# Performance work log

Hardware: AMD Instinct MI355X
Metric: run time of the kernel (lower is better)

## Reference

```python
import jax, jax.numpy as jnp
import numpy as np

B, S, D, H, E, KW = 2, 2048, 1024, 8, 128, 16  # batch, seq, d_model, heads, head_width, kernel_width


def setup_inputs() -> dict:
    key = jax.random.key(0)
    ks = jax.random.split(key, 10)
    sc = D ** -0.5
    x = jax.random.normal(ks[0], (B, S, D), dtype=jnp.float32)
    Wq = jax.random.normal(ks[1], (H, D, E), dtype=jnp.float32) * sc
    bq = jnp.zeros((H, E), dtype=jnp.float32)
    Wk = jax.random.normal(ks[2], (H, D, E), dtype=jnp.float32) * sc
    bk = jnp.zeros((H, E), dtype=jnp.float32)
    Wv = jax.random.normal(ks[3], (H, D, E), dtype=jnp.float32) * sc
    bv = jnp.zeros((H, E), dtype=jnp.float32)
    Wo = jax.random.normal(ks[4], (H, E, D), dtype=jnp.float32) * ((H * E) ** -0.5)
    bo = jnp.zeros((D,), dtype=jnp.float32)
    dilations = jnp.array([1, 1, 2, 2, 4, 4, 8, 8], dtype=jnp.int32)
    return {"x": x, "Wq": Wq, "bq": bq, "Wk": Wk, "bk": bk,
            "Wv": Wv, "bv": bv, "Wo": Wo, "bo": bo, "dilations": dilations}


def _windows(kh, vh, bkh, bvh, d):
    # kh, vh: [B, S, E] projected keys/values for one head; d: dilation (scalar int)
    s = kh.shape[1]
    # center-justified dilated window: positions i + d*j - d*(KW-1)//2
    pos = jnp.arange(s)[:, None] + d * jnp.arange(KW)[None, :] - (d * (KW - 1)) // 2
    valid = (pos >= 0) & (pos < s)            # [S, KW]
    posc = jnp.clip(pos, 0, s - 1)
    # padded positions hold the zero-embedding, whose projection is just the bias
    kw = jnp.where(valid[None, :, :, None], kh[:, posc, :], bkh)  # [B, S, KW, E]
    vw = jnp.where(valid[None, :, :, None], vh[:, posc, :], bvh)
    return kw, vw


def _lcsa(x, Wq, bq, Wk, bk, Wv, bv, Wo, bo, dilations):
    # per-head independent projections (Core.Linear with parallel shape [heads])
    q = jnp.einsum('bsd,hde->bhse', x, Wq) + bq[None, :, None, :]       # [B,H,S,E]
    k_all = jnp.einsum('bsd,hde->bhse', x, Wk) + bk[None, :, None, :]
    v_all = jnp.einsum('bsd,hde->bhse', x, Wv) + bv[None, :, None, :]
    # gather dilated local windows per head (project-then-gather; padded = bias)
    kw, vw = jax.vmap(_windows, in_axes=(1, 1, 0, 0, 0))(k_all, v_all, bk, bv, dilations)
    # kw, vw: [H, B, S, KW, E]
    logits = jnp.einsum('bhse,hbske->bhsk', q, kw)                       # [B,H,S,KW]
    score = jax.nn.softmax(logits, axis=-1)
    # NOTE: original divides by sqrt(d_head) AFTER softmax*value (faithful quirk)
    attn = jnp.einsum('bhsk,hbske->bhse', score, vw) / jnp.sqrt(jnp.asarray(E, x.dtype))
    out = jnp.einsum('bhse,hed->bsd', attn, Wo) + bo                     # dehead merge
    return out


def reference(x, Wq, bq, Wk, bk, Wv, bv, Wo, bo, dilations):
    return _lcsa(x, Wq, bq, Wk, bk, Wv, bv, Wo, bo, dilations)
```

## Files before the change

kernel.cpp:

```cpp
#include <hip/hip_runtime.h>
#include <stdint.h>

#define Bb 2
#define Ss 2048
#define Dd 1024
#define Hh 8
#define Ee 128
#define KWW 16
#define Mm (Bb*Ss)
#define Kk 1024

typedef unsigned short u16;
typedef __attribute__((ext_vector_type(8))) _Float16 f16x8;
typedef __attribute__((ext_vector_type(4))) float f32x4;

__device__ __forceinline__ u16 f2h(float f) {
  union { _Float16 h; u16 u; } v; v.h = (_Float16)f; return v.u;
}
__device__ __forceinline__ float h2f(u16 u) {
  union { u16 u; _Float16 h; } v; v.u = u; return (float)v.h;
}
__device__ __forceinline__ float h2f_lo(uint32_t w) { return h2f((u16)(w & 0xFFFF)); }
__device__ __forceinline__ float h2f_hi(uint32_t w) { return h2f((u16)(w >> 16)); }

__device__ __forceinline__ void gll16(const void* g, void* l) {
  __builtin_amdgcn_global_load_lds((const __attribute__((address_space(1))) void*)g,
                                   (__attribute__((address_space(3))) void*)l, 16, 0, 0);
}

__global__ __launch_bounds__(256) void prep(
    const float* __restrict__ x, const float* __restrict__ Wq,
    const float* __restrict__ Wk, const float* __restrict__ Wv,
    const float* __restrict__ Wo,
    u16* __restrict__ xh, u16* __restrict__ wT, u16* __restrict__ woT) {
  const int bid = blockIdx.x;
  const int tid = threadIdx.x;
  if (bid < 4096) {
    int i = (bid * 256 + tid) * 4;
    float4 f = *(const float4*)(x + i);
    uint64_t pk = (uint64_t)f2h(f.x) | ((uint64_t)f2h(f.y) << 16) |
                  ((uint64_t)f2h(f.z) << 32) | ((uint64_t)f2h(f.w) << 48);
    *(uint64_t*)(xh + i) = pk;
    return;
  }
  __shared__ float tile[32][33];
  const int tx = tid & 31, ty = tid >> 5;
  if (bid < 4096 + 3072) {
    const int idx = bid - 4096;
    const int z = idx >> 7, rem = idx & 127;
    const int h = z & 7;
    const float* W = (z < 8) ? Wq : (z < 16) ? Wk : Wv;
    const float* ib = W + (size_t)h * Dd * Ee;
    u16* ob = wT + (size_t)z * Ee * Kk;
    const int r0 = (rem & 31) * 32, c0 = (rem >> 5) * 32;
    #pragma unroll
    for (int kq = 0; kq < 4; kq++)
      tile[ty + 8*kq][tx] = ib[(size_t)(r0 + ty + 8*kq) * Ee + (c0 + tx)];
    __syncthreads();
    const int k = r0 + tx;
    #pragma unroll
    for (int kq = 0; kq < 4; kq++) {
      const int n = c0 + ty + 8*kq;
      ob[(((size_t)(k >> 3) * 128 + n) << 3) + (k & 7)] = f2h(tile[tx][ty + 8*kq]);
    }
  } else {
    const int idx = bid - (4096 + 3072);
    const int r0 = (idx & 31) * 32, c0 = (idx >> 5) * 32;
    const int C = Dd;
    #pragma unroll
    for (int kq = 0; kq < 4; kq++)
      tile[ty + 8*kq][tx] = Wo[(size_t)(r0 + ty + 8*kq) * C + (c0 + tx)];
    __syncthreads();
    const int k = r0 + tx;
    #pragma unroll
    for (int kq = 0; kq < 4; kq++) {
      const int n = c0 + ty + 8*kq;
      woT[(size_t)(n >> 7) * 131072 +
          (((size_t)(k >> 3) * 128 + (n & 127)) << 3) + (k & 7)] = f2h(tile[tx][ty + 8*kq]);
    }
  }
}

template<int MT>
__device__ __forceinline__ void gemm_core(
    const u16* __restrict__ A, const u16* __restrict__ Btf,
    u16* As, f32x4 (&acc)[MT / 32][4]) {
  constexpr int MI = MT / 32;
  const int tid = threadIdx.x;
  const int wave = tid >> 6;
  const int lane = tid & 63;
  const size_t lnoff = (size_t)(lane >> 3) * Kk + (size_t)(((lane & 7) ^ (lane >> 3)) * 8);

  const int wm = (wave >> 1) * (MT / 2);
  const int wn = (wave & 1) * 64;
  const int fr = lane & 15;
  const int q  = lane >> 4;
  const int sw = fr & 7;

  const u16* bptr = Btf + ((size_t)q * 128 + wn + fr) * 8;
  f16x8 bcur[8], bnxt[8];
  #pragma unroll
  for (int ks = 0; ks < 2; ks++)
    #pragma unroll
    for (int j = 0; j < 4; j++)
      bcur[ks * 4 + j] = *(const f16x8*)(bptr + (ks * 4) * 1024 + j * 128);

  #pragma unroll
  for (int i = 0; i < MI; i++)
    #pragma unroll
    for (int j = 0; j < 4; j++)
      #pragma unroll
      for (int r = 0; r < 4; r++) acc[i][j][r] = 0.0f;

  #pragma unroll
  for (int c = 0; c < MI; c++)
    gll16(A + lnoff + (size_t)((c * 4 + wave) * 8) * Kk, As + (c * 4 + wave) * 512);
  __syncthreads();

  for (int w = 0; w < Kk / 64; w++) {
    const int kt = w * 64;
    u16* cur = As + (w & 1) * (MT * 64);
    u16* nxt = As + ((w + 1) & 1) * (MT * 64);
    if (w + 1 < Kk / 64) {
      #pragma unroll
      for (int c = 0; c < MI; c++)
        gll16(A + lnoff + (size_t)((c * 4 + wave) * 8) * Kk + kt + 64, nxt + (c * 4 + wave) * 512);
    }
    const int ktn = (kt + 64) & (Kk - 1);
    #pragma unroll
    for (int ks = 0; ks < 2; ks++)
      #pragma unroll
      for (int j = 0; j < 4; j++)
        bnxt[ks * 4 + j] = *(const f16x8*)(bptr + ((ktn >> 3) + ks * 4) * 1024 + j * 128);
    #pragma unroll
    for (int ks = 0; ks < 2; ks++) {
      const int col = ((ks << 2) | q) ^ sw;
      f16x8 ah[MI];
      #pragma unroll
      for (int i = 0; i < MI; i++)
        ah[i] = *(const f16x8*)(cur + (wm + i * 16 + fr) * 64 + col * 8);
      #pragma unroll
      for (int i = 0; i < MI; i++)
        #pragma unroll
        for (int j = 0; j < 4; j++)
          acc[i][j] = __builtin_amdgcn_mfma_f32_16x16x32_f16(ah[i], bcur[ks * 4 + j], acc[i][j], 0, 0, 0);
    }
    __syncthreads();
    #pragma unroll
    for (int t = 0; t < 8; t++) bcur[t] = bnxt[t];
  }
}


__global__ __launch_bounds__(256) void gemm_qkv(
    const u16* __restrict__ xh, const u16* __restrict__ wT,
    const float* __restrict__ bq, const float* __restrict__ bk, const float* __restrict__ bv,
    u16* __restrict__ q, u16* __restrict__ k, u16* __restrict__ v) {
  __shared__ u16 As[128 * 64 * 2];
  const int m0 = blockIdx.x * 128;
  const int z = blockIdx.z;
  const int proj = z >> 3, h = z & 7;
  f32x4 acc[4][4];
  gemm_core<128>(xh + (size_t)m0 * Kk, wT + (size_t)z * (Ee * Kk), As, acc);

  u16* dst = proj == 0 ? q : (proj == 1 ? k : v);
  const float* bias = proj == 0 ? bq : (proj == 1 ? bk : bv);
  const int wave = threadIdx.x >> 6, lane = threadIdx.x & 63;
  const int wm = (wave >> 1) * 64, wn = (wave & 1) * 64;
  const int cn = lane & 15, rq4 = (lane >> 4) * 4;
  #pragma unroll
  for (int j = 0; j < 4; j++) {
    const int e = wn + j * 16 + cn;
    const float bb = bias[h * Ee + e];
    #pragma unroll
    for (int i = 0; i < 4; i++) {
      #pragma unroll
      for (int r = 0; r < 4; r++) {
        const int m = m0 + wm + i * 16 + rq4 + r;
        const int b = m >> 11, s = m & (Ss - 1);
        dst[(((size_t)(b * Hh + h)) * Ss + s) * Ee + e] = f2h(acc[i][j][r] + bb);
      }
    }
  }
}

__global__ __launch_bounds__(256) void gemm_out(
    const u16* __restrict__ attn, const u16* __restrict__ woT,
    const float* __restrict__ bo, float* __restrict__ out) {
  __shared__ u16 As[64 * 64 * 2];
  const int m0 = blockIdx.x * 64;
  const int n0 = blockIdx.y * 128;
  f32x4 acc[2][4];
  gemm_core<64>(attn + (size_t)m0 * Kk, woT + (size_t)blockIdx.y * 131072, As, acc);
  const int wave = threadIdx.x >> 6, lane = threadIdx.x & 63;
  const int wm = (wave >> 1) * 32, wn = (wave & 1) * 64;
  const int cn = lane & 15, rq4 = (lane >> 4) * 4;
  #pragma unroll
  for (int j = 0; j < 4; j++) {
    const int n = n0 + wn + j * 16 + cn;
    const float bb = bo[n];
    #pragma unroll
    for (int i = 0; i < 2; i++) {
      #pragma unroll
      for (int r = 0; r < 4; r++) {
        const int m = m0 + wm + i * 16 + rq4 + r;
        out[(size_t)m * Dd + n] = acc[i][j][r] + bb;
      }
    }
  }
}

__global__ __launch_bounds__(256) void attn_kernel(
    const u16* __restrict__ q, const u16* __restrict__ k, const u16* __restrict__ v,
    const float* __restrict__ bk, const float* __restrict__ bv,
    const int* __restrict__ dil, u16* __restrict__ attn) {
  const int nblk = (Bb * Hh * Ss) / 16;
  const int blk = (blockIdx.x & 7) * (nblk / 8) + (blockIdx.x >> 3);
  const int wid = blk * 4 + (threadIdx.x >> 6);
  const int lane = threadIdx.x & 63;
  const int grp = lane >> 4;
  const int lx = lane & 15;
  const int idx = wid * 4 + grp;
  const int s = idx & (Ss - 1);
  const int bh = idx >> 11;
  const int h = bh & 7, b = bh >> 3;
  const int d = dil[h];
  const size_t base = (size_t)bh * Ss * Ee;
  const u16* kp = k + base;
  const u16* vp = v + base;
  const int e0 = lx * 8;
  const int off = (d * (KWW - 1)) >> 1;

  float qf[8];
  {
    uint4 qw = *(const uint4*)(q + base + (size_t)s * Ee + e0);
    qf[0] = h2f_lo(qw.x); qf[1] = h2f_hi(qw.x);
    qf[2] = h2f_lo(qw.y); qf[3] = h2f_hi(qw.y);
    qf[4] = h2f_lo(qw.z); qf[5] = h2f_hi(qw.z);
    qf[6] = h2f_lo(qw.w); qf[7] = h2f_hi(qw.w);
  }
  float bkf[8], bvf[8];
  {
    const float4 a0 = ((const float4*)(bk + h * Ee + e0))[0];
    const float4 a1 = ((const float4*)(bk + h * Ee + e0))[1];
    bkf[0]=a0.x; bkf[1]=a0.y; bkf[2]=a0.z; bkf[3]=a0.w;
    bkf[4]=a1.x; bkf[5]=a1.y; bkf[6]=a1.z; bkf[7]=a1.w;
    const float4 c0 = ((const float4*)(bv + h * Ee + e0))[0];
    const float4 c1 = ((const float4*)(bv + h * Ee + e0))[1];
    bvf[0]=c0.x; bvf[1]=c0.y; bvf[2]=c0.z; bvf[3]=c0.w;
    bvf[4]=c1.x; bvf[5]=c1.y; bvf[6]=c1.z; bvf[7]=c1.w;
  }
  float blog = 0.f;
  #pragma unroll
  for (int i = 0; i < 8; i++) blog += qf[i] * bkf[i];
  uint4 bvh;
  bvh.x = (uint32_t)f2h(bvf[0]) | ((uint32_t)f2h(bvf[1]) << 16);
  bvh.y = (uint32_t)f2h(bvf[2]) | ((uint32_t)f2h(bvf[3]) << 16);
  bvh.z = (uint32_t)f2h(bvf[4]) | ((uint32_t)f2h(bvf[5]) << 16);
  bvh.w = (uint32_t)f2h(bvf[6]) | ((uint32_t)f2h(bvf[7]) << 16);

  float logit[KWW];
  #pragma unroll
  for (int j = 0; j < KWW; j++) {
    const int pos = s + d * j - off;
    const int posc = min(max(pos, 0), Ss - 1);
    uint4 kw = *(const uint4*)(kp + (size_t)posc * Ee + e0);
    float t = qf[0] * h2f_lo(kw.x) + qf[1] * h2f_hi(kw.x)
            + qf[2] * h2f_lo(kw.y) + qf[3] * h2f_hi(kw.y)
            + qf[4] * h2f_lo(kw.z) + qf[5] * h2f_hi(kw.z)
            + qf[6] * h2f_lo(kw.w) + qf[7] * h2f_hi(kw.w);
    logit[j] = (pos >= 0 && pos < Ss) ? t : blog;
  }

  uint4 vrow[KWW];
  #pragma unroll
  for (int j = 0; j < KWW; j++) {
    const int pos = s + d * j - off;
    const int posc = min(max(pos, 0), Ss - 1);
    uint4 vw = *(const uint4*)(vp + (size_t)posc * Ee + e0);
    const bool ok = (pos >= 0) && (pos < Ss);
    vrow[j].x = ok ? vw.x : bvh.x;
    vrow[j].y = ok ? vw.y : bvh.y;
    vrow[j].z = ok ? vw.z : bvh.z;
    vrow[j].w = ok ? vw.w : bvh.w;
  }

  {
    const bool hi = (lx & 8) != 0;
    #pragma unroll
    for (int jj = 0; jj < 8; jj++) {
      float send = hi ? logit[jj] : logit[jj + 8];
      float recv = __shfl_xor(send, 8, 64);
      logit[jj] = (hi ? logit[jj + 8] : logit[jj]) + recv;
    }
  }
  {
    const bool hi = (lx & 4) != 0;
    #pragma unroll
    for (int jj = 0; jj < 4; jj++) {
      float send = hi ? logit[jj] : logit[jj + 4];
      float recv = __shfl_xor(send, 4, 64);
      logit[jj] = (hi ? logit[jj + 4] : logit[jj]) + recv;
    }
  }
  {
    const bool hi = (lx & 2) != 0;
    #pragma unroll
    for (int jj = 0; jj < 2; jj++) {
      float send = hi ? logit[jj] : logit[jj + 2];
      float recv = __shfl_xor(send, 2, 64);
      logit[jj] = (hi ? logit[jj + 2] : logit[jj]) + recv;
    }
  }
  float own;
  {
    const bool hi = (lx & 1) != 0;
    float send = hi ? logit[0] : logit[1];
    float recv = __shfl_xor(send, 1, 64);
    own = (hi ? logit[1] : logit[0]) + recv;
  }

  float mx = own;
  mx = fmaxf(mx, __shfl_xor(mx, 1, 64));
  mx = fmaxf(mx, __shfl_xor(mx, 2, 64));
  mx = fmaxf(mx, __shfl_xor(mx, 4, 64));
  mx = fmaxf(mx, __shfl_xor(mx, 8, 64));
  float w = __expf(own - mx);
  float sum = w;
  sum += __shfl_xor(sum, 1, 64);
  sum += __shfl_xor(sum, 2, 64);
  sum += __shfl_xor(sum, 4, 64);
  sum += __shfl_xor(sum, 8, 64);
  w *= 1.0f / (sum * 11.313708498984760f);

  const int gbase = lane & 48;
  float gj[KWW];
  #pragma unroll
  for (int j = 0; j < KWW; j++)
    gj[j] = __shfl(w, gbase | j, 64);

  float acc[8];
  #pragma unroll
  for (int i = 0; i < 8; i++) acc[i] = 0.f;
  #pragma unroll
  for (int j = 0; j < KWW; j++) {
    const float wt = gj[j];
    acc[0] += wt * h2f_lo(vrow[j].x);
    acc[1] += wt * h2f_hi(vrow[j].x);
    acc[2] += wt * h2f_lo(vrow[j].y);
    acc[3] += wt * h2f_hi(vrow[j].y);
    acc[4] += wt * h2f_lo(vrow[j].z);
    acc[5] += wt * h2f_hi(vrow[j].z);
    acc[6] += wt * h2f_lo(vrow[j].w);
    acc[7] += wt * h2f_hi(vrow[j].w);
  }

  uint4 o;
  o.x = (uint32_t)f2h(acc[0]) | ((uint32_t)f2h(acc[1]) << 16);
  o.y = (uint32_t)f2h(acc[2]) | ((uint32_t)f2h(acc[3]) << 16);
  o.z = (uint32_t)f2h(acc[4]) | ((uint32_t)f2h(acc[5]) << 16);
  o.w = (uint32_t)f2h(acc[6]) | ((uint32_t)f2h(acc[7]) << 16);
  *(uint4*)(attn + (size_t)(b * Ss + s) * (Hh * Ee) + h * Ee + e0) = o;
}

extern "C" void kernel_launch(void* const* d_in, const int* in_sizes, int n_in,
                              void* d_out, int out_size, void* d_ws, size_t ws_size,
                              hipStream_t stream) {
  (void)in_sizes; (void)n_in; (void)out_size; (void)ws_size;
  const float* x  = (const float*)d_in[0];
  const float* Wq = (const float*)d_in[1];
  const float* bq = (const float*)d_in[2];
  const float* Wk = (const float*)d_in[3];
  const float* bk = (const float*)d_in[4];
  const float* Wv = (const float*)d_in[5];
  const float* bv = (const float*)d_in[6];
  const float* Wo = (const float*)d_in[7];
  const float* bo = (const float*)d_in[8];
  const int* dil  = (const int*)d_in[9];
  float* out = (float*)d_out;

  char* ws = (char*)d_ws;
  u16* xh  = (u16*)ws;  ws += (size_t)Mm * Kk * 2;
  u16* wT  = (u16*)ws;  ws += (size_t)24 * Ee * Kk * 2;
  u16* woT = (u16*)ws;  ws += (size_t)Kk * Dd * 2;
  u16* q = (u16*)ws; ws += (size_t)Bb * Hh * Ss * Ee * 2;
  u16* k = (u16*)ws; ws += (size_t)Bb * Hh * Ss * Ee * 2;
  u16* v = (u16*)ws; ws += (size_t)Bb * Hh * Ss * Ee * 2;
  u16* attn = xh;

  prep<<<8192, 256, 0, stream>>>(x, Wq, Wk, Wv, Wo, xh, wT, woT);
  gemm_qkv<<<dim3(Mm / 128, 1, 24), 256, 0, stream>>>(xh, wT, bq, bk, bv, q, k, v);
  attn_kernel<<<(Bb * Hh * Ss) / 16, 256, 0, stream>>>(q, k, v, bk, bv, dil, attn);
  gemm_out<<<dim3(Mm / 64, Dd / 128), 256, 0, stream>>>(attn, woT, bo, out);
}
```

Baseline: 155.9 us.

## Triple-buffer A tiles in GEMM core with explicit vmcnt waits

The shared GEMM core moves from a double-buffered LDS A tile with a full __syncthreads per step to a three-stage ring. Global-to-LDS loads run two K-steps ahead, and each step waits with a partial s_waitcnt vmcnt so only the oldest tile must have landed before the barrier. This aims to hide global load latency behind the MFMA work and avoid draining all outstanding loads each iteration. In exchange it uses more LDS, which may lower occupancy, and correctness now depends on hand-counted vmcnt values matching the compiler's issued loads.

```diff
diff --git a/kernel.cpp b/kernel.cpp
--- a/kernel.cpp
+++ b/kernel.cpp
@@ -86,6 +86,8 @@
     const u16* __restrict__ A, const u16* __restrict__ Btf,
     u16* As, f32x4 (&acc)[MT / 32][4]) {
   constexpr int MI = MT / 32;
+  constexpr int SZ = MT * 64;
+  constexpr int NW = Kk / 64;
   const int tid = threadIdx.x;
   const int wave = tid >> 6;
   const int lane = tid & 63;
@@ -99,6 +101,13 @@
 
   const u16* bptr = Btf + ((size_t)q * 128 + wn + fr) * 8;
   f16x8 bcur[8], bnxt[8];
+
+  #pragma unroll
+  for (int c = 0; c < MI; c++)
+    gll16(A + lnoff + (size_t)((c * 4 + wave) * 8) * Kk, As + (c * 4 + wave) * 512);
+  #pragma unroll
+  for (int c = 0; c < MI; c++)
+    gll16(A + lnoff + (size_t)((c * 4 + wave) * 8) * Kk + 64, As + SZ + (c * 4 + wave) * 512);
   #pragma unroll
   for (int ks = 0; ks < 2; ks++)
     #pragma unroll
@@ -112,40 +121,54 @@
       #pragma unroll
       for (int r = 0; r < 4; r++) acc[i][j][r] = 0.0f;
 
-  #pragma unroll
-  for (int c = 0; c < MI; c++)
-    gll16(A + lnoff + (size_t)((c * 4 + wave) * 8) * Kk, As + (c * 4 + wave) * 512);
-  __syncthreads();
-
-  for (int w = 0; w < Kk / 64; w++) {
-    const int kt = w * 64;
-    u16* cur = As + (w & 1) * (MT * 64);
-    u16* nxt = As + ((w + 1) & 1) * (MT * 64);
-    if (w + 1 < Kk / 64) {
-      #pragma unroll
-      for (int c = 0; c < MI; c++)
-        gll16(A + lnoff + (size_t)((c * 4 + wave) * 8) * Kk + kt + 64, nxt + (c * 4 + wave) * 512);
-    }
-    const int ktn = (kt + 64) & (Kk - 1);
+  if constexpr (MT == 128) {
+    asm volatile("s_waitcnt vmcnt(12) lgkmcnt(0)" ::: "memory");
+  } else {
+    asm volatile("s_waitcnt vmcnt(10) lgkmcnt(0)" ::: "memory");
+  }
+  __builtin_amdgcn_s_barrier();
+
+  u16* p0 = As;
+  u16* p1 = As + SZ;
+  u16* p2 = As + 2 * SZ;
+
+  for (int w = 0; w < NW; w++) {
+    const int ktn = ((w + 1) * 64) & (Kk - 1);
     #pragma unroll
     for (int ks = 0; ks < 2; ks++)
       #pragma unroll
       for (int j = 0; j < 4; j++)
         bnxt[ks * 4 + j] = *(const f16x8*)(bptr + ((ktn >> 3) + ks * 4) * 1024 + j * 128);
+    if (w + 2 < NW) {
+      #pragma unroll
+      for (int c = 0; c < MI; c++)
+        gll16(A + lnoff + (size_t)((c * 4 + wave) * 8) * Kk + (size_t)(w + 2) * 64,
+              p2 + (c * 4 + wave) * 512);
+    }
     #pragma unroll
     for (int ks = 0; ks < 2; ks++) {
       const int col = ((ks << 2) | q) ^ sw;
       f16x8 ah[MI];
       #pragma unroll
       for (int i = 0; i < MI; i++)
-        ah[i] = *(const f16x8*)(cur + (wm + i * 16 + fr) * 64 + col * 8);
+        ah[i] = *(const f16x8*)(p0 + (wm + i * 16 + fr) * 64 + col * 8);
       #pragma unroll
       for (int i = 0; i < MI; i++)
         #pragma unroll
         for (int j = 0; j < 4; j++)
           acc[i][j] = __builtin_amdgcn_mfma_f32_16x16x32_f16(ah[i], bcur[ks * 4 + j], acc[i][j], 0, 0, 0);
     }
-    __syncthreads();
+    if (w < NW - 1) {
+      if (w == NW - 2) {
+        asm volatile("s_waitcnt vmcnt(8) lgkmcnt(0)" ::: "memory");
+      } else if constexpr (MT == 128) {
+        asm volatile("s_waitcnt vmcnt(12) lgkmcnt(0)" ::: "memory");
+      } else {
+        asm volatile("s_waitcnt vmcnt(10) lgkmcnt(0)" ::: "memory");
+      }
+      __builtin_amdgcn_s_barrier();
+    }
+    u16* tp = p0; p0 = p1; p1 = p2; p2 = tp;
     #pragma unroll
     for (int t = 0; t < 8; t++) bcur[t] = bnxt[t];
   }
@@ -156,7 +179,7 @@
     const u16* __restrict__ xh, const u16* __restrict__ wT,
     const float* __restrict__ bq, const float* __restrict__ bk, const float* __restrict__ bv,
     u16* __restrict__ q, u16* __restrict__ k, u16* __restrict__ v) {
-  __shared__ u16 As[128 * 64 * 2];
+  __shared__ u16 As[128 * 64 * 3];
   const int m0 = blockIdx.x * 128;
   const int z = blockIdx.z;
   const int proj = z >> 3, h = z & 7;
@@ -187,7 +210,7 @@
 __global__ __launch_bounds__(256) void gemm_out(
     const u16* __restrict__ attn, const u16* __restrict__ woT,
     const float* __restrict__ bo, float* __restrict__ out) {
-  __shared__ u16 As[64 * 64 * 2];
+  __shared__ u16 As[64 * 64 * 3];
   const int m0 = blockIdx.x * 64;
   const int n0 = blockIdx.y * 128;
   f32x4 acc[2][4];
```

After: 163.9 us. 1.05x slower.
